# Kernel tuning notes

Measured on AMD Instinct MI355X. Metric: run time of the kernel, lower is better.

The kernel has to match this reference:

```python
import jax, jax.numpy as jnp
import numpy as np

B = 512      # batch
K = 16       # nm_operators
SD = 64      # subspace_dim = v_dim / nm_operators
T = 64       # timesteps


def setup_inputs() -> dict:
    key = jax.random.key(0)
    k1, k2, k3 = jax.random.split(key, 3)
    u_t = jax.random.normal(k1, (B, K), dtype=jnp.float32)
    s_t = jax.random.normal(k2, (B, K, 2 * SD), dtype=jnp.float32)
    # orthogonal init (gain sqrt(2)) per operator, like init.orthogonal_
    g = jax.random.normal(k3, (K, 2 * SD, 2 * SD), dtype=jnp.float32)
    q, _ = jnp.linalg.qr(g)
    H = q * np.float32(np.sqrt(2.0))
    return {"u_t": u_t, "s_t": s_t, "H": H, "timesteps": T, "startidx": 0}


def _matrix_exp(X, order=10):
    # Taylor-series matrix exponential, order 10 (per-operator identity)
    n = X.shape[-1]
    I = jnp.broadcast_to(jnp.eye(n, dtype=X.dtype), X.shape)
    out = I
    power = I
    for i in range(order):
        power = jnp.matmul(power, X) / jnp.asarray(i + 1.0, X.dtype)
        out = out + power
    return out


def _hamiltonian(H):
    # A = sym(H); Hm = S @ A with S = [[0, I], [-I, 0]]
    K_, D2, _ = H.shape
    D = D2 // 2
    A = 0.5 * (H + jnp.swapaxes(H, 1, 2))            # [K, 2D, 2D]
    J = jnp.eye(D, dtype=H.dtype)
    Z = jnp.zeros((D, D), dtype=H.dtype)
    S = jnp.block([[Z, J], [-J, Z]])                 # [2D, 2D]
    return jnp.einsum('ik,nkj->nij', S, A)           # [K, 2D, 2D]


def reference(u_t, s_t, H, timesteps, startidx):
    # dynamics='Hamiltonian', condnU=True, projection=True, startidx=0
    expH = _matrix_exp(_hamiltonian(H))              # [K, 2D, 2D]

    def step(s, _):
        s2 = jnp.einsum('kid,bkd->bki', expH, s)     # per-operator propagation
        return s2, s2

    _, rest = jax.lax.scan(step, s_t, None, length=timesteps - 1)  # [T-1,B,K,2D]
    seq = jnp.concatenate([s_t[None], rest], axis=0)               # [T,B,K,2D]
    seq = jnp.moveaxis(seq, 0, 1)                                  # [B,T,K,2D]
    labels = jnp.argmax(u_t, axis=1)                               # [B]
    mask = jax.nn.one_hot(labels, H.shape[0], dtype=seq.dtype)     # [B,K]
    return seq * mask[:, None, :, None]
```

## Files before the change

kernel.cpp:

```cpp
#include <hip/hip_runtime.h>

#define BATCH  512
#define K_OPS  16
#define D2     128
#define TSTEPS 64

#define TAYB   256
#define ZK1    1024
#define CHAINB 512
#define ZK2    2048

typedef float vf4 __attribute__((ext_vector_type(4)));

__device__ inline int argmax16(const float* __restrict__ ub) {
    float m = ub[0]; int lab = 0;
    #pragma unroll
    for (int j = 1; j < K_OPS; ++j) {
        const float v = ub[j];
        if (v > m) { m = v; lab = j; }
    }
    return lab;
}

__global__ __launch_bounds__(256) void k_xbuild(
    const float* __restrict__ H, const float* __restrict__ u,
    float* __restrict__ X, int* __restrict__ labels)
{
    __shared__ float Hs[D2][132];
    const int k = blockIdx.x, tid = threadIdx.x;

    if (tid < 32) labels[k * 32 + tid] = argmax16(u + (k * 32 + tid) * K_OPS);

    const float* Hk = H + (size_t)k * D2 * D2;
    #pragma unroll
    for (int mm = 0; mm < 16; ++mm) {
        const int idx4 = tid + mm * 256;
        const float4 v = *(const float4*)&Hk[idx4 * 4];
        *(float4*)&Hs[idx4 >> 5][(idx4 & 31) * 4] = v;
    }
    __syncthreads();

    float* Xk = X + (size_t)k * D2 * D2;
    #pragma unroll 4
    for (int m = 0; m < 64; ++m) {
        const int idx = tid + m * 256;
        const int i = idx >> 7, j = idx & 127;
        const int i2 = i ^ 64;
        const float sgn = (i < 64) ? 0.5f : -0.5f;
        Xk[idx] = sgn * (Hs[i2][j] + Hs[j][i2]);
    }
}

__global__ __launch_bounds__(256, 2) void k_taylor(
    const float* __restrict__ X, float* __restrict__ ACC,
    float* __restrict__ out)
{
    const int bid = blockIdx.x, tid = threadIdx.x;

    if (bid >= TAYB) {
        const int zb = bid - TAYB;
        const vf4 zv = {0.f, 0.f, 0.f, 0.f};
        vf4* base = (vf4*)(out + (size_t)zb * 16 * 2048);
        #pragma unroll 4
        for (int s = 0; s < 16; ++s) {
            vf4* p = base + (size_t)s * 512;
            p[tid]       = zv;
            p[tid + 256] = zv;
        }
        return;
    }

    __shared__ float PsT[D2][12];
    __shared__ float Red[3][64][20];

    const int k   = bid >> 4;
    const int r0s = (bid & 15) * 8;
    const float* Xk = X + (size_t)k * D2 * D2;

    const int jg = tid >> 6;
    const int rg = (tid >> 5) & 1;
    const int cg = tid & 31;

    float x[32][4];
    #pragma unroll
    for (int m = 0; m < 32; ++m) {
        const int j = (m << 2) | jg;
        const float4 a = *(const float4*)&Xk[j * D2 + cg * 4];
        x[m][0] = a.x; x[m][1] = a.y; x[m][2] = a.z; x[m][3] = a.w;
    }

    {
        const int c = tid & 127, rh = tid >> 7;
        float4 v; float* vp = (float*)&v;
        #pragma unroll
        for (int rr = 0; rr < 4; ++rr)
            vp[rr] = Xk[(r0s + rh * 4 + rr) * D2 + c];
        *(float4*)&PsT[c][rh * 4] = v;
    }

    float acc[4][4];
    if (jg == 0) {
        #pragma unroll
        for (int rr = 0; rr < 4; ++rr) {
            const int row = r0s + rg * 4 + rr;
            const float4 a = *(const float4*)&Xk[row * D2 + cg * 4];
            acc[rr][0] = a.x + ((row == cg * 4 + 0) ? 1.0f : 0.0f);
            acc[rr][1] = a.y + ((row == cg * 4 + 1) ? 1.0f : 0.0f);
            acc[rr][2] = a.z + ((row == cg * 4 + 2) ? 1.0f : 0.0f);
            acc[rr][3] = a.w + ((row == cg * 4 + 3) ? 1.0f : 0.0f);
        }
    }
    __syncthreads();

    for (int it = 2; it <= 10; ++it) {
        float nv[4][4] = {{0.f,0.f,0.f,0.f},{0.f,0.f,0.f,0.f},
                          {0.f,0.f,0.f,0.f},{0.f,0.f,0.f,0.f}};
        #pragma unroll
        for (int m = 0; m < 32; ++m) {
            const int j = (m << 2) | jg;
            const float4 pv = *(const float4*)&PsT[j][rg * 4];
            const float p[4] = {pv.x, pv.y, pv.z, pv.w};
            #pragma unroll
            for (int rr = 0; rr < 4; ++rr)
                #pragma unroll
                for (int cc = 0; cc < 4; ++cc)
                    nv[rr][cc] = fmaf(p[rr], x[m][cc], nv[rr][cc]);
        }
        if (jg != 0) {
            float* rb = Red[jg - 1][rg * 32 + cg];
            #pragma unroll
            for (int rr = 0; rr < 4; ++rr)
                *(float4*)&rb[rr * 4] =
                    make_float4(nv[rr][0], nv[rr][1], nv[rr][2], nv[rr][3]);
        }
        __syncthreads();
        if (jg == 0) {
            #pragma unroll
            for (int g = 0; g < 3; ++g) {
                const float* rb = Red[g][rg * 32 + cg];
                #pragma unroll
                for (int rr = 0; rr < 4; ++rr) {
                    const float4 p = *(const float4*)&rb[rr * 4];
                    nv[rr][0] += p.x; nv[rr][1] += p.y;
                    nv[rr][2] += p.z; nv[rr][3] += p.w;
                }
            }
            const float inv = 1.0f / (float)it;
            #pragma unroll
            for (int rr = 0; rr < 4; ++rr)
                #pragma unroll
                for (int cc = 0; cc < 4; ++cc) {
                    nv[rr][cc] *= inv;
                    acc[rr][cc] += nv[rr][cc];
                }
            #pragma unroll
            for (int cc = 0; cc < 4; ++cc)
                *(float4*)&PsT[cg * 4 + cc][rg * 4] =
                    make_float4(nv[0][cc], nv[1][cc], nv[2][cc], nv[3][cc]);
        }
        __syncthreads();
    }

    if (jg == 0) {
        float* Ak = ACC + ((size_t)k * D2 + r0s + rg * 4) * D2;
        #pragma unroll
        for (int rr = 0; rr < 4; ++rr)
            *(float4*)&Ak[rr * D2 + cg * 4] =
                make_float4(acc[rr][0], acc[rr][1], acc[rr][2], acc[rr][3]);
    }
}

__global__ __launch_bounds__(128, 2) void k_prop(
    const float* __restrict__ s_in, const float* __restrict__ ACC,
    const int* __restrict__ labels, float* __restrict__ out)
{
    const int bid = blockIdx.x, tid = threadIdx.x;

    if (bid >= CHAINB) {
        const int z = bid - CHAINB;
        const int b = 256 + (z >> 3);
        const int sub = z & 7;
        const int lab = labels[b];
        const vf4 zv = {0.f, 0.f, 0.f, 0.f};
        vf4* base = (vf4*)(out + ((size_t)b * TSTEPS + sub * 8) * (K_OPS * D2));
        #pragma unroll 4
        for (int s = 0; s < 8; ++s) {
            vf4* p = base + (size_t)s * 512;
            #pragma unroll
            for (int q = 0; q < 4; ++q) {
                const int slot = tid + q * 128;
                if ((slot >> 5) != lab) p[slot] = zv;
            }
        }
        return;
    }

    __shared__ float sbuf[D2];
    __shared__ float shipA[64];
    __shared__ float shipB[64];

    const int jh = tid >> 6;
    const int l  = tid & 63;
    const int b  = bid;
    const int lab = labels[b];

    float rlo[64], rhi[64];
    {
        const float4* pl = (const float4*)(ACC + ((size_t)lab * D2 + l) * D2 + jh * 64);
        const float4* ph = (const float4*)(ACC + ((size_t)lab * D2 + l + 64) * D2 + jh * 64);
        #pragma unroll
        for (int q = 0; q < 16; ++q) {
            const float4 a = pl[q];
            rlo[4*q+0] = a.x; rlo[4*q+1] = a.y; rlo[4*q+2] = a.z; rlo[4*q+3] = a.w;
            const float4 c = ph[q];
            rhi[4*q+0] = c.x; rhi[4*q+1] = c.y; rhi[4*q+2] = c.z; rhi[4*q+3] = c.w;
        }
    }

    const float s0 = s_in[((size_t)b * K_OPS + lab) * D2 + tid];
    sbuf[tid] = s0;
    float* ob = out + ((size_t)b * TSTEPS * K_OPS + lab) * D2;
    ob[tid] = s0;
    asm volatile("s_waitcnt lgkmcnt(0)\n\ts_barrier" ::: "memory");

    for (int t = 1; t < TSTEPS; ++t) {
        float p0 = 0.f, p1 = 0.f;
        const float4* s4 = (const float4*)&sbuf[jh * 64];
        #pragma unroll
        for (int q = 0; q < 16; ++q) {
            const float4 sv = s4[q];
            p0 = fmaf(rlo[4*q+0], sv.x, p0);
            p0 = fmaf(rlo[4*q+1], sv.y, p0);
            p0 = fmaf(rlo[4*q+2], sv.z, p0);
            p0 = fmaf(rlo[4*q+3], sv.w, p0);
            p1 = fmaf(rhi[4*q+0], sv.x, p1);
            p1 = fmaf(rhi[4*q+1], sv.y, p1);
            p1 = fmaf(rhi[4*q+2], sv.z, p1);
            p1 = fmaf(rhi[4*q+3], sv.w, p1);
        }
        if (jh == 0) shipA[l] = p1; else shipB[l] = p0;
        asm volatile("s_waitcnt lgkmcnt(0)\n\ts_barrier" ::: "memory");
        const float mine  = (jh == 0) ? p0 : p1;
        const float other = (jh == 0) ? shipB[l] : shipA[l];
        const float y = mine + other;
        sbuf[tid] = y;
        ob[(size_t)t * (K_OPS * D2) + tid] = y;
        asm volatile("s_waitcnt lgkmcnt(0)\n\ts_barrier" ::: "memory");
    }
}

extern "C" void kernel_launch(void* const* d_in, const int* in_sizes, int n_in,
                              void* d_out, int out_size, void* d_ws, size_t ws_size,
                              hipStream_t stream) {
    const float* u_t = (const float*)d_in[0];
    const float* s_t = (const float*)d_in[1];
    const float* H   = (const float*)d_in[2];

    float* out    = (float*)d_out;
    float* Xw     = (float*)d_ws;
    float* Aw     = Xw + K_OPS * D2 * D2;
    int*   labels = (int*)(Aw + K_OPS * D2 * D2);

    hipLaunchKernelGGL(k_xbuild, dim3(K_OPS), dim3(256), 0, stream,
                       H, u_t, Xw, labels);
    hipLaunchKernelGGL(k_taylor, dim3(TAYB + ZK1), dim3(256), 0, stream,
                       Xw, Aw, out);
    hipLaunchKernelGGL(k_prop, dim3(CHAINB + ZK2), dim3(128), 0, stream,
                       s_t, Aw, labels, out);
}
```

Measured before the change: 71.33 us.

## Fold zero-fill blocks into chain blocks as extra waves overlapping recurrence

```diff
diff --git a/kernel.cpp b/kernel.cpp
--- a/kernel.cpp
+++ b/kernel.cpp
@@ -8,9 +8,10 @@
 #define TAYB   256
 #define ZK1    1024
 #define CHAINB 512
-#define ZK2    2048
 
 typedef float vf4 __attribute__((ext_vector_type(4)));
+
+#define ASM_BAR() asm volatile("s_waitcnt lgkmcnt(0)\n\ts_barrier" ::: "memory")
 
 __device__ inline int argmax16(const float* __restrict__ ub) {
     float m = ub[0]; int lab = 0;
@@ -170,42 +171,32 @@
     }
 }
 
-__global__ __launch_bounds__(128, 2) void k_prop(
+__global__ void k_prop(
     const float* __restrict__ s_in, const float* __restrict__ ACC,
     const int* __restrict__ labels, float* __restrict__ out)
 {
     const int bid = blockIdx.x, tid = threadIdx.x;
-
-    if (bid >= CHAINB) {
-        const int z = bid - CHAINB;
-        const int b = 256 + (z >> 3);
-        const int sub = z & 7;
-        const int lab = labels[b];
-        const vf4 zv = {0.f, 0.f, 0.f, 0.f};
-        vf4* base = (vf4*)(out + ((size_t)b * TSTEPS + sub * 8) * (K_OPS * D2));
-        #pragma unroll 4
-        for (int s = 0; s < 8; ++s) {
-            vf4* p = base + (size_t)s * 512;
-            #pragma unroll
-            for (int q = 0; q < 4; ++q) {
-                const int slot = tid + q * 128;
-                if ((slot >> 5) != lab) p[slot] = zv;
-            }
-        }
-        return;
-    }
+    const int wv = tid >> 6;
+    const bool chainw = (wv < 2);
 
     __shared__ float sbuf[D2];
     __shared__ float shipA[64];
     __shared__ float shipB[64];
 
-    const int jh = tid >> 6;
+    const int lab = labels[bid];
+
+    const int zb   = 256 + (bid >> 1);
+    const int zlab = labels[zb];
+    float* zbase = out + ((size_t)zb * TSTEPS + (size_t)(bid & 1) * 32) * (K_OPS * D2);
+    const int zl = tid & 127;
+    const vf4 zv = {0.f, 0.f, 0.f, 0.f};
+
+    const int jh = wv;
     const int l  = tid & 63;
-    const int b  = bid;
-    const int lab = labels[b];
-
     float rlo[64], rhi[64];
-    {
+    float* ob = out + ((size_t)bid * TSTEPS * K_OPS + lab) * D2;
+
+    if (chainw) {
         const float4* pl = (const float4*)(ACC + ((size_t)lab * D2 + l) * D2 + jh * 64);
         const float4* ph = (const float4*)(ACC + ((size_t)lab * D2 + l + 64) * D2 + jh * 64);
         #pragma unroll
@@ -215,37 +206,53 @@
             const float4 c = ph[q];
             rhi[4*q+0] = c.x; rhi[4*q+1] = c.y; rhi[4*q+2] = c.z; rhi[4*q+3] = c.w;
         }
-    }
-
-    const float s0 = s_in[((size_t)b * K_OPS + lab) * D2 + tid];
-    sbuf[tid] = s0;
-    float* ob = out + ((size_t)b * TSTEPS * K_OPS + lab) * D2;
-    ob[tid] = s0;
-    asm volatile("s_waitcnt lgkmcnt(0)\n\ts_barrier" ::: "memory");
+        const float s0 = s_in[((size_t)bid * K_OPS + lab) * D2 + tid];
+        sbuf[tid] = s0;
+        ob[tid] = s0;
+    }
+    ASM_BAR();
 
     for (int t = 1; t < TSTEPS; ++t) {
         float p0 = 0.f, p1 = 0.f;
-        const float4* s4 = (const float4*)&sbuf[jh * 64];
-        #pragma unroll
-        for (int q = 0; q < 16; ++q) {
-            const float4 sv = s4[q];
-            p0 = fmaf(rlo[4*q+0], sv.x, p0);
-            p0 = fmaf(rlo[4*q+1], sv.y, p0);
-            p0 = fmaf(rlo[4*q+2], sv.z, p0);
-            p0 = fmaf(rlo[4*q+3], sv.w, p0);
-            p1 = fmaf(rhi[4*q+0], sv.x, p1);
-            p1 = fmaf(rhi[4*q+1], sv.y, p1);
-            p1 = fmaf(rhi[4*q+2], sv.z, p1);
-            p1 = fmaf(rhi[4*q+3], sv.w, p1);
-        }
-        if (jh == 0) shipA[l] = p1; else shipB[l] = p0;
-        asm volatile("s_waitcnt lgkmcnt(0)\n\ts_barrier" ::: "memory");
-        const float mine  = (jh == 0) ? p0 : p1;
-        const float other = (jh == 0) ? shipB[l] : shipA[l];
-        const float y = mine + other;
-        sbuf[tid] = y;
-        ob[(size_t)t * (K_OPS * D2) + tid] = y;
-        asm volatile("s_waitcnt lgkmcnt(0)\n\ts_barrier" ::: "memory");
+        if (chainw) {
+            const float4* s4 = (const float4*)&sbuf[jh * 64];
+            #pragma unroll
+            for (int q = 0; q < 16; ++q) {
+                const float4 sv = s4[q];
+                p0 = fmaf(rlo[4*q+0], sv.x, p0);
+                p0 = fmaf(rlo[4*q+1], sv.y, p0);
+                p0 = fmaf(rlo[4*q+2], sv.z, p0);
+                p0 = fmaf(rlo[4*q+3], sv.w, p0);
+                p1 = fmaf(rhi[4*q+0], sv.x, p1);
+                p1 = fmaf(rhi[4*q+1], sv.y, p1);
+                p1 = fmaf(rhi[4*q+2], sv.z, p1);
+                p1 = fmaf(rhi[4*q+3], sv.w, p1);
+            }
+            if (jh == 0) shipA[l] = p1; else shipB[l] = p0;
+        } else {
+            const int c = t - 1;
+            vf4* p = (vf4*)(zbase + (size_t)(c >> 1) * 2048);
+            const int s1 = ((c & 1) << 8) + zl;
+            const int s2 = s1 + 128;
+            if ((s1 >> 5) != zlab) p[s1] = zv;
+            if ((s2 >> 5) != zlab) p[s2] = zv;
+        }
+        ASM_BAR();
+        if (chainw) {
+            const float mine  = (jh == 0) ? p0 : p1;
+            const float other = (jh == 0) ? shipB[l] : shipA[l];
+            const float y = mine + other;
+            sbuf[tid] = y;
+            ob[(size_t)t * (K_OPS * D2) + tid] = y;
+        } else if (t == 1) {
+            const int c = 63;
+            vf4* p = (vf4*)(zbase + (size_t)(c >> 1) * 2048);
+            const int s1 = ((c & 1) << 8) + zl;
+            const int s2 = s1 + 128;
+            if ((s1 >> 5) != zlab) p[s1] = zv;
+            if ((s2 >> 5) != zlab) p[s2] = zv;
+        }
+        ASM_BAR();
     }
 }
 
@@ -265,6 +272,6 @@
                        H, u_t, Xw, labels);
     hipLaunchKernelGGL(k_taylor, dim3(TAYB + ZK1), dim3(256), 0, stream,
                        Xw, Aw, out);
-    hipLaunchKernelGGL(k_prop, dim3(CHAINB + ZK2), dim3(128), 0, stream,
+    hipLaunchKernelGGL(k_prop, dim3(CHAINB), dim3(256), 0, stream,
                        s_t, Aw, labels, out);
 }
```

Measured after the change: 137.1 us. 92.3% more time.

## Split propagation matvec across four waves with shared-memory reduction

Applied to the files above, without the earlier changes.

```diff
diff --git a/kernel.cpp b/kernel.cpp
--- a/kernel.cpp
+++ b/kernel.cpp
@@ -6,11 +6,13 @@
 #define TSTEPS 64
 
 #define TAYB   256
-#define ZK1    1024
+#define ZK1    832
 #define CHAINB 512
-#define ZK2    2048
+#define ZK2    2432
 
 typedef float vf4 __attribute__((ext_vector_type(4)));
+
+#define ASM_BAR() asm volatile("s_waitcnt lgkmcnt(0)\n\ts_barrier" ::: "memory")
 
 __device__ inline int argmax16(const float* __restrict__ ub) {
     float m = ub[0]; int lab = 0;
@@ -170,7 +172,7 @@
     }
 }
 
-__global__ __launch_bounds__(128, 2) void k_prop(
+__global__ __launch_bounds__(256, 2) void k_prop(
     const float* __restrict__ s_in, const float* __restrict__ ACC,
     const int* __restrict__ labels, float* __restrict__ out)
 {
@@ -178,7 +180,7 @@
 
     if (bid >= CHAINB) {
         const int z = bid - CHAINB;
-        const int b = 256 + (z >> 3);
+        const int b = 208 + (z >> 3);
         const int sub = z & 7;
         const int lab = labels[b];
         const vf4 zv = {0.f, 0.f, 0.f, 0.f};
@@ -187,8 +189,8 @@
         for (int s = 0; s < 8; ++s) {
             vf4* p = base + (size_t)s * 512;
             #pragma unroll
-            for (int q = 0; q < 4; ++q) {
-                const int slot = tid + q * 128;
+            for (int q = 0; q < 2; ++q) {
+                const int slot = tid + q * 256;
                 if ((slot >> 5) != lab) p[slot] = zv;
             }
         }
@@ -196,56 +198,59 @@
     }
 
     __shared__ float sbuf[D2];
-    __shared__ float shipA[64];
-    __shared__ float shipB[64];
-
-    const int jh = tid >> 6;
-    const int l  = tid & 63;
-    const int b  = bid;
+    __shared__ float part[4][132];
+
+    const int q = tid >> 6;
+    const int l = tid & 63;
+    const int b = bid;
     const int lab = labels[b];
 
-    float rlo[64], rhi[64];
+    float rA[32], rB[32];
     {
-        const float4* pl = (const float4*)(ACC + ((size_t)lab * D2 + l) * D2 + jh * 64);
-        const float4* ph = (const float4*)(ACC + ((size_t)lab * D2 + l + 64) * D2 + jh * 64);
-        #pragma unroll
-        for (int q = 0; q < 16; ++q) {
-            const float4 a = pl[q];
-            rlo[4*q+0] = a.x; rlo[4*q+1] = a.y; rlo[4*q+2] = a.z; rlo[4*q+3] = a.w;
-            const float4 c = ph[q];
-            rhi[4*q+0] = c.x; rhi[4*q+1] = c.y; rhi[4*q+2] = c.z; rhi[4*q+3] = c.w;
-        }
-    }
-
-    const float s0 = s_in[((size_t)b * K_OPS + lab) * D2 + tid];
-    sbuf[tid] = s0;
+        const float4* pl = (const float4*)(ACC + ((size_t)lab * D2 + l) * D2 + q * 32);
+        const float4* ph = (const float4*)(ACC + ((size_t)lab * D2 + l + 64) * D2 + q * 32);
+        #pragma unroll
+        for (int m = 0; m < 8; ++m) {
+            const float4 a = pl[m];
+            rA[4*m+0] = a.x; rA[4*m+1] = a.y; rA[4*m+2] = a.z; rA[4*m+3] = a.w;
+            const float4 c = ph[m];
+            rB[4*m+0] = c.x; rB[4*m+1] = c.y; rB[4*m+2] = c.z; rB[4*m+3] = c.w;
+        }
+    }
+
     float* ob = out + ((size_t)b * TSTEPS * K_OPS + lab) * D2;
-    ob[tid] = s0;
-    asm volatile("s_waitcnt lgkmcnt(0)\n\ts_barrier" ::: "memory");
+    if (tid < D2) {
+        const float s0 = s_in[((size_t)b * K_OPS + lab) * D2 + tid];
+        sbuf[tid] = s0;
+        ob[tid] = s0;
+    }
+    ASM_BAR();
 
     for (int t = 1; t < TSTEPS; ++t) {
         float p0 = 0.f, p1 = 0.f;
-        const float4* s4 = (const float4*)&sbuf[jh * 64];
-        #pragma unroll
-        for (int q = 0; q < 16; ++q) {
-            const float4 sv = s4[q];
-            p0 = fmaf(rlo[4*q+0], sv.x, p0);
-            p0 = fmaf(rlo[4*q+1], sv.y, p0);
-            p0 = fmaf(rlo[4*q+2], sv.z, p0);
-            p0 = fmaf(rlo[4*q+3], sv.w, p0);
-            p1 = fmaf(rhi[4*q+0], sv.x, p1);
-            p1 = fmaf(rhi[4*q+1], sv.y, p1);
-            p1 = fmaf(rhi[4*q+2], sv.z, p1);
-            p1 = fmaf(rhi[4*q+3], sv.w, p1);
-        }
-        if (jh == 0) shipA[l] = p1; else shipB[l] = p0;
-        asm volatile("s_waitcnt lgkmcnt(0)\n\ts_barrier" ::: "memory");
-        const float mine  = (jh == 0) ? p0 : p1;
-        const float other = (jh == 0) ? shipB[l] : shipA[l];
-        const float y = mine + other;
-        sbuf[tid] = y;
-        ob[(size_t)t * (K_OPS * D2) + tid] = y;
-        asm volatile("s_waitcnt lgkmcnt(0)\n\ts_barrier" ::: "memory");
+        const float4* s4 = (const float4*)&sbuf[q * 32];
+        #pragma unroll
+        for (int m = 0; m < 8; ++m) {
+            const float4 sv = s4[m];
+            p0 = fmaf(rA[4*m+0], sv.x, p0);
+            p0 = fmaf(rA[4*m+1], sv.y, p0);
+            p0 = fmaf(rA[4*m+2], sv.z, p0);
+            p0 = fmaf(rA[4*m+3], sv.w, p0);
+            p1 = fmaf(rB[4*m+0], sv.x, p1);
+            p1 = fmaf(rB[4*m+1], sv.y, p1);
+            p1 = fmaf(rB[4*m+2], sv.z, p1);
+            p1 = fmaf(rB[4*m+3], sv.w, p1);
+        }
+        part[q][l]      = p0;
+        part[q][64 + l] = p1;
+        ASM_BAR();
+        if (q < 2) {
+            const int r = q * 64 + l;
+            const float y = part[0][r] + part[1][r] + part[2][r] + part[3][r];
+            sbuf[r] = y;
+            ob[(size_t)t * (K_OPS * D2) + r] = y;
+        }
+        ASM_BAR();
     }
 }
 
@@ -265,6 +270,6 @@
                        H, u_t, Xw, labels);
     hipLaunchKernelGGL(k_taylor, dim3(TAYB + ZK1), dim3(256), 0, stream,
                        Xw, Aw, out);
-    hipLaunchKernelGGL(k_prop, dim3(CHAINB + ZK2), dim3(128), 0, stream,
+    hipLaunchKernelGGL(k_prop, dim3(CHAINB + ZK2), dim3(256), 0, stream,
                        s_t, Aw, labels, out);
 }
```

After: 61.48 us. 13.8% less time.
